# Optimization experiments

Hardware: AMD Instinct MI355X
Metric: run time of the kernel (lower is better)

Reference implementation:

```python
import jax, jax.numpy as jnp
import numpy as np
from jax import lax

N = 1024  # n_nodes


def _gumbel(key, shape, eps=1e-10):
    u = jax.random.uniform(key, shape)
    return -jnp.log(-jnp.log(u + eps) + eps)


def setup_inputs() -> dict:
    key = jax.random.key(0)
    k1, k2, k3, k4 = jax.random.split(key, 4)
    root_probs = jax.random.uniform(k1, (N,), dtype=jnp.float32)
    edge_probs = jax.random.uniform(k2, (N, N), dtype=jnp.float32)
    g_roots = _gumbel(k3, (N, 2))
    g_edges = _gumbel(k4, (N, N, 2))
    return {"root_probs": root_probs, "edge_probs": edge_probs,
            "g_roots": g_roots, "g_edges": g_edges}


def _st_gumbel0(logit0, logit1, g):
    """Hard gumbel-softmax over the 2-vector [logit0, logit1]; returns
    (straight-through value of component 0, hard boolean of component 0).
    tau = 1 (torch default). softmax over 2 elems == sigmoid of diff."""
    z0 = logit0 + g[..., 0]
    z1 = logit1 + g[..., 1]
    soft0 = jax.nn.sigmoid(z0 - z1)
    hard0 = z0 > z1
    st0 = hard0.astype(soft0.dtype) + soft0 - lax.stop_gradient(soft0)
    return st0, hard0


def reference(root_probs, edge_probs, g_roots, g_edges):
    n = root_probs.shape[0]
    f32 = root_probs.dtype
    # root indicators (straight-through) -- roots_one_hot in the original
    roots_st, root_hard = _st_gumbel0(root_probs, 1.0 - root_probs, g_roots)
    # all potential edge samples (straight-through), row i consumed when node i is processed
    st_e, hard_e = _st_gumbel0(edge_probs, 1.0 - edge_probs, g_edges)

    idx = jnp.arange(n, dtype=jnp.int32)
    # initial FIFO queue = root nodes in ascending order; slot n is a scratch slot
    pos = jnp.cumsum(root_hard.astype(jnp.int32)) - 1
    queue0 = jnp.zeros((n + 1,), jnp.int32).at[jnp.where(root_hard, pos, n)].set(idx)
    tail0 = jnp.sum(root_hard.astype(jnp.int32))
    anc0 = jnp.eye(n, dtype=bool)        # anc[k] = ancestor set of node k (incl. k)
    inq0 = root_hard                      # enqueued-once mask (dedupe == 'sampled' skip)

    not_root_f = 1.0 - roots_st           # differentiable via straight-through
    not_root_b = ~root_hard

    def step(carry, _):
        anc, queue, head, tail, inq = carry
        active = head < tail
        i = queue[jnp.where(active, head, n)]          # scratch slot holds 0
        anc_i = anc[i]                                  # (n,) bool
        # candidates = (1 - roots_one_hot) * (not an ancestor of i)
        cand = not_root_f * (1.0 - anc_i.astype(f32))
        row = st_e[i] * cand                            # dag row i
        # forward value of dag[i, j] == 1  <=>  hard edge & hard candidate
        hit = hard_e[i] & not_root_b & (~anc_i) & active
        # ancestors[j] |= ancestors[i] | {i}  (anc_i already contains i)
        anc = jnp.where(hit[:, None], anc | anc_i[None, :], anc)
        # enqueue newly hit nodes (each node enqueued/processed at most once)
        new = hit & (~inq)
        pos2 = jnp.cumsum(new.astype(jnp.int32)) - 1
        queue = queue.at[jnp.where(new, tail + pos2, n)].set(idx)
        inq = inq | new
        tail = tail + jnp.sum(new.astype(jnp.int32))
        head = head + active.astype(jnp.int32)
        row = jnp.where(active, row, jnp.zeros_like(row))
        return (anc, queue, head, tail, inq), (i, row)

    init = (anc0, queue0, jnp.int32(0), tail0, inq0)
    _, (i_seq, rows) = lax.scan(step, init, None, length=n)
    # scatter processed rows into dag (each real i appears once; idle steps add zeros)
    dag = jnp.zeros((n, n), f32).at[i_seq].add(rows)
    return dag
```

## Files before the change

kernel.cpp:

```cpp
#include <hip/hip_runtime.h>

#define NN 1024
#define NW 32
#define KMAX 640
#define KW 10
#define AP  13
#define BTP 11
#define NBIN 1024

typedef unsigned int u32;
typedef unsigned long long u64;
typedef unsigned short u16;

__device__ __forceinline__ u64 rdl64(u64 v, int s) {
    u32 lo = (u32)__builtin_amdgcn_readlane((int)(u32)v, s);
    u32 hi = (u32)__builtin_amdgcn_readlane((int)(u32)(v >> 32), s);
    return ((u64)hi << 32) | (u64)lo;
}
__device__ __forceinline__ u64 bitmask64(u64 x, int s) {
    return (u64)(((long long)(x << (63 - s))) >> 63);
}

__global__ void edge_bits_kernel(const float* __restrict__ ep, const float* __restrict__ ge,
                                 u32* __restrict__ E)
{
    int idx = blockIdx.x * blockDim.x + threadIdx.x;
    float p = ep[idx];
    float2 g = reinterpret_cast<const float2*>(ge)[idx];
    bool hard = (p + g.x) > ((1.0f - p) + g.y);
    u64 m = __ballot(hard);
    int lane = threadIdx.x & 63;
    if ((lane & 31) == 0) E[idx >> 5] = (u32)(m >> (lane & 32));
}

__global__ __launch_bounds__(1024) void seed_kernel(
    const float* __restrict__ rp, const float* __restrict__ gr,
    const u32* __restrict__ Eg, u32* __restrict__ meta_g,
    u16* __restrict__ posof_g, u16* __restrict__ npl_g)
{
    extern __shared__ u32 sd[];
    u32* hist  = sd;
    u32* scan  = hist + NBIN * 16;
    u32* wtot  = scan + NBIN;
    u32* rootm = wtot + 16;
    u16* rlist = (u16*)(rootm + 32);

    const int tid = threadIdx.x;
    const int lane = tid & 63;
    const int wid  = tid >> 6;

    float p0 = rp[tid];
    float2 g0 = reinterpret_cast<const float2*>(gr)[tid];
    bool isroot = (p0 + g0.x) > ((1.0f - p0) + g0.y);
    u64 rm = __ballot(isroot);
    if (lane == 0) { rootm[wid * 2] = (u32)rm; rootm[wid * 2 + 1] = (u32)(rm >> 32); }
    for (int i = tid; i < NBIN * 16; i += 1024) hist[i] = 0u;
    __syncthreads();

    int rb = 0, nroots = 0;
    {
        const int myw = tid >> 5;
        const u32 mybitm = (1u << (tid & 31)) - 1u;
        #pragma unroll
        for (int w = 0; w < 32; ++w) {
            u32 m = rootm[w];
            int pc = __popc(m);
            nroots += pc;
            rb += (myw > w) ? pc : ((myw == w) ? __popc(m & mybitm) : 0);
        }
    }
    if (isroot) rlist[rb] = (u16)tid;
    __syncthreads();

    int fr = -1;
    if (!isroot) {
        const int mywd = tid >> 5;
        const u32 mybit = 1u << (tid & 31);
        for (int b = 0; b < nroots; b += 4) {
            u32 w0 = 0, w1 = 0, w2 = 0, w3 = 0;
            int n = nroots - b;
            w0 = Eg[(size_t)rlist[b] * NW + mywd];
            if (n > 1) w1 = Eg[(size_t)rlist[b + 1] * NW + mywd];
            if (n > 2) w2 = Eg[(size_t)rlist[b + 2] * NW + mywd];
            if (n > 3) w3 = Eg[(size_t)rlist[b + 3] * NW + mywd];
            if (fr < 0 && (w0 & mybit)) fr = b;
            if (fr < 0 && (w1 & mybit)) fr = b + 1;
            if (fr < 0 && (w2 & mybit)) fr = b + 2;
            if (fr < 0 && (w3 & mybit)) fr = b + 3;
            if (__all(fr >= 0)) break;
        }
    }
    bool found = (!isroot) && (fr >= 0);
    u32 ridx = found ? (u32)fr : 0xFFFFFFFFu;

    if (found) atomicAdd(&hist[ridx * 16 + wid], 1u);
    __syncthreads();

    u32 v;
    {
        const uint4* h4 = (const uint4*)(hist + tid * 16);
        uint4 a = h4[0], b = h4[1], c = h4[2], d = h4[3];
        v = a.x + a.y + a.z + a.w + b.x + b.y + b.z + b.w
          + c.x + c.y + c.z + c.w + d.x + d.y + d.z + d.w;
    }
    #pragma unroll
    for (int d2 = 1; d2 < 64; d2 <<= 1) {
        u32 u = (u32)__shfl_up((int)v, d2);
        if (lane >= d2) v += u;
    }
    if (lane == 63) wtot[wid] = v;
    __syncthreads();
    {
        u32 off = 0;
        #pragma unroll
        for (int w2 = 0; w2 < 16; ++w2) off += (w2 < wid) ? wtot[w2] : 0u;
        v += off;
        scan[tid] = v;
    }
    __syncthreads();

    int intra = 0;
    #pragma unroll 64
    for (int l2 = 0; l2 < 64; ++l2) {
        u32 rr = (u32)__builtin_amdgcn_readlane((int)ridx, l2);
        intra += (rr == ridx && l2 < lane) ? 1 : 0;
    }
    u32 pos = 0;
    if (found) {
        u32 base = (ridx > 0) ? scan[ridx - 1] : 0u;
        u32 wb = 0;
        for (int w = 0; w < wid; ++w) wb += hist[ridx * 16 + w];
        pos = base + wb + (u32)intra;
        if (pos < KMAX) npl_g[pos] = (u16)tid;
    }
    posof_g[tid] = isroot ? (u16)0xFFFF : (found ? (u16)pos : (u16)1023);
    if (tid == 0) {
        u32 tl = scan[NBIN - 1];
        meta_g[0] = (tl < (u32)KMAX) ? tl : (u32)KMAX;
    }
}

__global__ __launch_bounds__(256) void transposeB_kernel(
    const u32* __restrict__ E, const u16* __restrict__ npl_g,
    const u32* __restrict__ meta_g, u64* __restrict__ BT_g)
{
    __shared__ u16 npL[KMAX];
    const int tid = threadIdx.x;
    for (int k = tid; k < KMAX; k += 256) npL[k] = npl_g[k];
    u32 tail = meta_g[0];
    __syncthreads();
    int wseq = (blockIdx.x * 256 + tid) >> 6;
    int lane = tid & 63;
    int t = wseq / KW, w = wseq - t * KW;
    if (t >= (int)tail) return;
    int jt = npL[t];
    int s = w * 64 + lane;
    u32 ev = 0;
    if (s < (int)tail) {
        int is = npL[s];
        ev = (E[(size_t)is * NW + (jt >> 5)] >> (jt & 31)) & 1u;
    }
    u64 m = __ballot(ev != 0);
    if (lane == 0) BT_g[wseq] = m;
}

__global__ __launch_bounds__(1024) void bfs_closure(
    const u64* __restrict__ BT_g, u64* __restrict__ A_g, const u32* __restrict__ meta_g)
{
    extern __shared__ u64 sm[];
    u64* A   = sm;
    u64* BTL = A + KMAX * AP;

    const int tid  = threadIdx.x;
    const int lane = tid & 63;
    const int wid  = tid >> 6;
    const int tail = (int)meta_g[0];
    const int nb   = (tail + 63) >> 6;

    for (int r = tid; r < tail; r += 1024) {
        const u64* src = BT_g + (size_t)r * KW;
        u64* dst = BTL + (size_t)r * BTP;
        #pragma unroll
        for (int w = 0; w < KW; ++w) dst[w] = src[w];
    }
    for (int r = tid; r < tail; r += 1024) {
        u64* dst = A + (size_t)r * AP;
        #pragma unroll
        for (int w = 0; w < AP; ++w) dst[w] = (w == (r >> 6)) ? (1ull << (r & 63)) : 0ull;
    }
    __syncthreads();

    for (int p = 0; p < nb; ++p) {
        if (wid <= p) {
            __builtin_amdgcn_s_setprio(1);
            const int t = (p << 6) + lane;
            const bool valid = t < tail;
            u64 av = valid ? A[(size_t)t * AP + wid] : ~0ull;
            if (!__all(av == ~0ull)) {
                if (wid < p) {
                    u64 asrc = A[(size_t)(((p - 1) << 6) + lane) * AP + wid];
                    u64 xb = valid ? BTL[(size_t)t * BTP + (p - 1)] : 0ull;
                    #pragma unroll 64
                    for (int s = 0; s < 64; ++s)
                        av |= rdl64(asrc, s) & bitmask64(xb, s);
                }
                if (!__all(av == ~0ull)) {
                    u64 xd = valid ? BTL[(size_t)t * BTP + p] : 0ull;
                    xd &= (1ull << lane) - 1ull;
                    #pragma unroll 63
                    for (int s = 0; s < 63; ++s)
                        av |= rdl64(av, s) & bitmask64(xd, s);
                }
                if (valid) A[(size_t)t * AP + wid] = av;
            }
            __builtin_amdgcn_s_setprio(0);
        } else if (p >= 1) {
            const int nbf = nb - 1 - p;
            const int C = p * nbf;
            const int nworkers = 15 - p;
            const int sb0 = (p - 1) << 6;
            for (int c = wid - p - 1; c < C; c += nworkers) {
                const int q = c / p;
                const int w = c - q * p;
                const int t = ((p + 1 + q) << 6) + lane;
                const bool valid = t < tail;
                u64 av = valid ? A[(size_t)t * AP + w] : ~0ull;
                if (!__all(av == ~0ull)) {
                    u64 asrc = A[(size_t)(sb0 + lane) * AP + w];
                    u64 x = valid ? BTL[(size_t)t * BTP + (p - 1)] : 0ull;
                    #pragma unroll 64
                    for (int s = 0; s < 64; ++s)
                        av |= rdl64(asrc, s) & bitmask64(x, s);
                    if (valid) A[(size_t)t * AP + w] = av;
                }
            }
        }
        __syncthreads();
    }

    for (int r = tid; r < tail; r += 1024) {
        const u64* src = A + (size_t)r * AP;
        u64* dst = A_g + (size_t)r * KW;
        #pragma unroll
        for (int w = 0; w < KW; ++w) dst[w] = src[w];
    }
}

__global__ __launch_bounds__(256) void final_expand(
    const u32* __restrict__ E, const u64* __restrict__ A_g,
    const u16* __restrict__ posof_g, const u32* __restrict__ meta_g,
    float4* __restrict__ out)
{
    int gid = blockIdx.x * 256 + threadIdx.x;
    int i = gid >> 8;
    int j0 = (gid & 255) << 2;
    u32 tail = meta_g[0];
    u32 pi = posof_g[i];
    float r[4] = {0.f, 0.f, 0.f, 0.f};
    if (pi == 0xFFFFu) {
        u32 wv = E[(size_t)i * NW + (j0 >> 5)];
        #pragma unroll
        for (int t = 0; t < 4; ++t) {
            u32 pj = posof_g[j0 + t];
            bool nz = ((wv >> ((j0 & 31) + t)) & 1u) && (pj != 0xFFFFu);
            r[t] = nz ? 1.0f : 0.0f;
        }
    } else if (pi < tail) {
        const u64* Arow = A_g + (size_t)pi * KW;
        u32 wv = E[(size_t)i * NW + (j0 >> 5)];
        #pragma unroll
        for (int t = 0; t < 4; ++t) {
            u32 pj = posof_g[j0 + t];
            bool eb = (wv >> ((j0 & 31) + t)) & 1u;
            if (eb && pj != 0xFFFFu) {
                u64 ab = (pj < (u32)KMAX) ? Arow[pj >> 6] : 0ull;
                r[t] = ((ab >> (pj & 63)) & 1ull) ? 0.0f : 1.0f;
            }
        }
    }
    out[gid] = make_float4(r[0], r[1], r[2], r[3]);
}

extern "C" void kernel_launch(void* const* d_in, const int* in_sizes, int n_in,
                              void* d_out, int out_size, void* d_ws, size_t ws_size,
                              hipStream_t stream) {
    const float* root_probs = (const float*)d_in[0];
    const float* edge_probs = (const float*)d_in[1];
    const float* g_roots    = (const float*)d_in[2];
    const float* g_edges    = (const float*)d_in[3];

    char* ws = (char*)d_ws;
    u32* E       = (u32*)(ws);
    u64* BT_g    = (u64*)(ws + 131072);
    u64* A_g     = (u64*)(ws + 182272);
    u16* posof_g = (u16*)(ws + 233472);
    u16* npl_g   = (u16*)(ws + 235520);
    u32* meta_g  = (u32*)(ws + 236800);

    edge_bits_kernel<<<NN * NN / 256, 256, 0, stream>>>(edge_probs, g_edges, E);

    size_t lds_seed = (size_t)(NBIN * 16 + NBIN + 16 + 32) * 4 + NN * 2;
    hipFuncSetAttribute((const void*)seed_kernel,
                        hipFuncAttributeMaxDynamicSharedMemorySize, (int)lds_seed);
    seed_kernel<<<1, NN, lds_seed, stream>>>(root_probs, g_roots, E, meta_g, posof_g, npl_g);

    transposeB_kernel<<<KMAX * KW * 64 / 256, 256, 0, stream>>>(E, npl_g, meta_g, BT_g);

    size_t lds = (size_t)KMAX * AP * 8 + (size_t)KMAX * BTP * 8;
    hipFuncSetAttribute((const void*)bfs_closure,
                        hipFuncAttributeMaxDynamicSharedMemorySize, (int)lds);
    bfs_closure<<<1, NN, lds, stream>>>(BT_g, A_g, meta_g);

    final_expand<<<NN * NN / 4 / 256, 256, 0, stream>>>(E, A_g, posof_g, meta_g,
                                                        (float4*)d_out);
}
```

Baseline: 62.05 us.

## Process four wavefronts of edges per wave, widen histogram clear, reuse closure source rows

The edge-bit kernel now has each wave handle four consecutive 64-element chunks in an unrolled loop, with a quarter as many blocks launched, to cut launch and scheduling overhead on the bandwidth-bound pass. The seed kernel clears its LDS histogram with 64-bit stores instead of 32-bit ones. In the BFS closure, the work index is remapped so consecutive chunks for a wave share the same word column, which lets the source row from A be cached in a register and reloaded only when the column changes. The remap changes the order in which chunks are assigned to waves, which may alter load balance.

New measurement: 61.61 us. Within noise of the previous version (-0.7%).

```diff
diff --git a/kernel.cpp b/kernel.cpp
--- a/kernel.cpp
+++ b/kernel.cpp
@@ -21,16 +21,21 @@
     return (u64)(((long long)(x << (63 - s))) >> 63);
 }
 
-__global__ void edge_bits_kernel(const float* __restrict__ ep, const float* __restrict__ ge,
-                                 u32* __restrict__ E)
-{
-    int idx = blockIdx.x * blockDim.x + threadIdx.x;
-    float p = ep[idx];
-    float2 g = reinterpret_cast<const float2*>(ge)[idx];
-    bool hard = (p + g.x) > ((1.0f - p) + g.y);
-    u64 m = __ballot(hard);
-    int lane = threadIdx.x & 63;
-    if ((lane & 31) == 0) E[idx >> 5] = (u32)(m >> (lane & 32));
+__global__ __launch_bounds__(256) void edge_bits_kernel(
+    const float* __restrict__ ep, const float* __restrict__ ge, u32* __restrict__ E)
+{
+    const int lane = threadIdx.x & 63;
+    const int wavebase = blockIdx.x * 1024 + (threadIdx.x >> 6) * 256;
+    #pragma unroll
+    for (int k = 0; k < 4; ++k) {
+        int e = wavebase + k * 64 + lane;
+        float p = ep[e];
+        float2 g = reinterpret_cast<const float2*>(ge)[e];
+        bool hard = (p + g.x) > ((1.0f - p) + g.y);
+        u64 m = __ballot(hard);
+        if ((lane & 31) == 0)
+            E[(wavebase >> 5) + k * 2 + (lane >> 5)] = (u32)(m >> (lane & 32));
+    }
 }
 
 __global__ __launch_bounds__(1024) void seed_kernel(
@@ -54,7 +59,10 @@
     bool isroot = (p0 + g0.x) > ((1.0f - p0) + g0.y);
     u64 rm = __ballot(isroot);
     if (lane == 0) { rootm[wid * 2] = (u32)rm; rootm[wid * 2 + 1] = (u32)(rm >> 32); }
-    for (int i = tid; i < NBIN * 16; i += 1024) hist[i] = 0u;
+    {
+        u64* h64 = (u64*)hist;
+        for (int i = tid; i < NBIN * 8; i += 1024) h64[i] = 0ull;
+    }
     __syncthreads();
 
     int rb = 0, nroots = 0;
@@ -219,14 +227,16 @@
             const int C = p * nbf;
             const int nworkers = 15 - p;
             const int sb0 = (p - 1) << 6;
+            int lastw = -1;
+            u64 asrc = 0;
             for (int c = wid - p - 1; c < C; c += nworkers) {
-                const int q = c / p;
-                const int w = c - q * p;
+                const int w = c / nbf;
+                const int q = c - w * nbf;
                 const int t = ((p + 1 + q) << 6) + lane;
                 const bool valid = t < tail;
                 u64 av = valid ? A[(size_t)t * AP + w] : ~0ull;
                 if (!__all(av == ~0ull)) {
-                    u64 asrc = A[(size_t)(sb0 + lane) * AP + w];
+                    if (w != lastw) { asrc = A[(size_t)(sb0 + lane) * AP + w]; lastw = w; }
                     u64 x = valid ? BTL[(size_t)t * BTP + (p - 1)] : 0ull;
                     #pragma unroll 64
                     for (int s = 0; s < 64; ++s)
@@ -297,7 +307,7 @@
     u16* npl_g   = (u16*)(ws + 235520);
     u32* meta_g  = (u32*)(ws + 236800);
 
-    edge_bits_kernel<<<NN * NN / 256, 256, 0, stream>>>(edge_probs, g_edges, E);
+    edge_bits_kernel<<<NN * NN / 1024, 256, 0, stream>>>(edge_probs, g_edges, E);
 
     size_t lds_seed = (size_t)(NBIN * 16 + NBIN + 16 + 32) * 4 + NN * 2;
     hipFuncSetAttribute((const void*)seed_kernel,
```
